# Optimization experiments

Measured on AMD Instinct MI355X. Metric: run time of the kernel, lower is better.

## Reference

```python
import jax, jax.numpy as jnp
import numpy as np

B, C_IN, FH, FW = 4, 256, 64, 176
N_PTS = 150000
D_BINS = 64
BEV_H = BEV_W = 200
RES = 0.5
EPS = 1e-5


def setup_inputs() -> dict:
    key = jax.random.key(0)
    ks = jax.random.split(key, 8)
    camera_features = jax.random.normal(ks[0], (B, C_IN, FH, FW), dtype=jnp.float32)
    pixels_uv = jax.random.uniform(ks[1], (B, N_PTS, 2), dtype=jnp.float32)
    K_inv = jax.random.normal(ks[2], (B, 3, 3), dtype=jnp.float32)
    # depth head params: Conv2d(256,128,3,pad=1) -> BN(128) -> ReLU -> Conv2d(128,64,1)
    W1 = jax.random.normal(ks[3], (128, C_IN, 3, 3), dtype=jnp.float32) * 0.02
    b1 = jnp.zeros((128,), dtype=jnp.float32)
    gamma = jnp.ones((128,), dtype=jnp.float32)
    beta = jnp.zeros((128,), dtype=jnp.float32)
    W2 = jax.random.normal(ks[4], (D_BINS, 128, 1, 1), dtype=jnp.float32) * 0.05
    b2 = jnp.zeros((D_BINS,), dtype=jnp.float32)
    depth_bins = jnp.linspace(1.0, 60.0, D_BINS, dtype=jnp.float32)
    return {"camera_features": camera_features, "pixels_uv": pixels_uv, "K_inv": K_inv,
            "W1": W1, "b1": b1, "gamma": gamma, "beta": beta, "W2": W2, "b2": b2,
            "depth_bins": depth_bins}


def _depth_head(x, W1, b1, gamma, beta, W2, b2):
    dn = ("NCHW", "OIHW", "NCHW")
    h = jax.lax.conv_general_dilated(x, W1, (1, 1), ((1, 1), (1, 1)), dimension_numbers=dn)
    h = h + b1[None, :, None, None]
    # BatchNorm2d, training-mode batch statistics (module is used without eval())
    mu = h.mean(axis=(0, 2, 3), keepdims=True)
    var = h.var(axis=(0, 2, 3), keepdims=True)
    h = (h - mu) * jax.lax.rsqrt(var + EPS)
    h = h * gamma[None, :, None, None] + beta[None, :, None, None]
    h = jax.nn.relu(h)
    logits = jax.lax.conv_general_dilated(h, W2, (1, 1), ((0, 0), (0, 0)), dimension_numbers=dn)
    logits = logits + b2[None, :, None, None]
    return jax.nn.softmax(logits, axis=1)  # [B, D, H, W]


def reference(camera_features, pixels_uv, K_inv, W1, b1, gamma, beta, W2, b2, depth_bins):
    depth_dist = _depth_head(camera_features, W1, b1, gamma, beta, W2, b2)

    # lift_to_3d
    exp_d = depth_dist.mean(axis=1)  # [B, H, W]
    ones = jnp.ones((B, N_PTS, 1), dtype=pixels_uv.dtype)
    homo = jnp.concatenate([pixels_uv, ones], axis=-1)            # [B, N, 3]
    pts3d = jnp.einsum('bnk,bjk->bnj', homo, K_inv)               # homo @ K_inv^T
    depth = exp_d.mean(axis=(1, 2))[:, None, None]                # [B, 1, 1]
    pts3d = pts3d * depth                                         # [B, N, 3]

    # splat_to_bev: scatter-add occupancy, then clamp to [0, 1]
    x_min = -(BEV_H * RES / 2)
    gx = jnp.clip(((pts3d[:, :, 0] - x_min) / RES).astype(jnp.int32), 0, BEV_W - 1)
    gy = jnp.clip(((pts3d[:, :, 1] - x_min) / RES).astype(jnp.int32), 0, BEV_H - 1)
    flat_idx = (jnp.arange(B, dtype=jnp.int32)[:, None] * (BEV_H * BEV_W) + gy * BEV_W + gx).ravel()
    grid = jnp.zeros((B * BEV_H * BEV_W,), dtype=jnp.float32).at[flat_idx].add(1.0)
    bev_grid = jnp.clip(grid.reshape(B, BEV_H, BEV_W), 0.0, 1.0)

    # expected_depth
    exp_depth = (depth_dist * depth_bins[None, :, None, None]).sum(axis=1)  # [B, H, W]

    return bev_grid, depth_dist, exp_depth, pts3d
```

## Files before the change

### kernel.cpp

```cpp
#include <hip/hip_runtime.h>

#define BATCH 4
#define CIN 256
#define FH 64
#define FW 176
#define HW (FH*FW)
#define PHW 11748
#define C1 128
#define DBINS 64
#define NPTS 150000
#define BEVN 200
#define EPSV 1e-5f

#define OFF_BEV 0
#define OFF_DD  160000
#define OFF_ED  3043584
#define OFF_PTS 3088640

#define WSB_H    0
#define WSB_WT   11534336
#define WSB_W2B  12124160
#define WSB_BN   12140544
#define WSB_XTP  12144640
#define XTP_B_ELEMS 3007488
#define WS_NEED_SPLIT 24174592ull

typedef short bfx8 __attribute__((ext_vector_type(8)));
typedef short bfx4 __attribute__((ext_vector_type(4)));
typedef float f32x4 __attribute__((ext_vector_type(4)));
typedef unsigned short u16;

__device__ __forceinline__ u16 f2bf(float f) {
  union { float f; unsigned int u; } v; v.f = f;
  unsigned int r = v.u + 0x7FFF + ((v.u >> 16) & 1);
  return (u16)(r >> 16);
}
__device__ __forceinline__ float bf2f(u16 h) {
  union { unsigned int u; float f; } v; v.u = ((unsigned int)h) << 16;
  return v.f;
}

__device__ __forceinline__ void gload_lds16(const void* g, void* l) {
  __builtin_amdgcn_global_load_lds(
      (const __attribute__((address_space(1))) unsigned int*)g,
      (__attribute__((address_space(3))) unsigned int*)l, 16, 0, 0);
}

__device__ __forceinline__ u16* xtp_base(u16* A, u16* B, int splitA, int bloc) {
  return (bloc < splitA) ? A + (size_t)bloc * XTP_B_ELEMS
                         : B + (size_t)(bloc - splitA) * XTP_B_ELEMS;
}

__global__ __launch_bounds__(256) void k_xt(
    const float* __restrict__ x, u16* __restrict__ xtpA,
    u16* __restrict__ xtpB, int splitA, int nbat,
    float* __restrict__ out, u16* __restrict__ w2b,
    const float* __restrict__ W2, u16* __restrict__ wt,
    const float* __restrict__ W1) {
  __shared__ u16 s_t[176 * 72];
  const int blk = blockIdx.x;
  const int t = threadIdx.x;
  const int idx = blk * 256 + t;

  if (idx < BATCH * BEVN * BEVN) out[OFF_BEV + idx] = 0.0f;
  if (idx < DBINS * C1) w2b[idx] = f2bf(W2[idx]);
  for (int i = idx; i < 9 * C1 * CIN; i += 262144) {
    int tap = i >> 15, rem = i & 32767;
    int co = rem >> 8, c = rem & 255;
    wt[i] = f2bf(W1[(co * CIN + c) * 9 + tap]);
  }
  const int nbord = nbat * 484 * 32;
  if (idx < nbord) {
    int bloc = idx / (484 * 32);
    int r = idx - bloc * 484 * 32;
    int bpx = r >> 5, ch8 = r & 31;
    int prow, pcol;
    if (bpx < 178)      { prow = 0;  pcol = bpx; }
    else if (bpx < 356) { prow = 65; pcol = bpx - 178; }
    else { int q = bpx - 356; prow = 1 + (q >> 1); pcol = (q & 1) * 177; }
    u16* xb = xtp_base(xtpA, xtpB, splitA, bloc);
    *(bfx8*)&xb[(prow * 178 + pcol) * 256 + ch8 * 8] = (bfx8)(short)0;
  }

  const int bloc = blk >> 8;
  const int rem = blk & 255;
  const int row = rem >> 2;
  const int c0 = (rem & 3) * 64;
  #pragma unroll
  for (int i = 0; i < 44; ++i) {
    int f = i * 256 + t;
    int c = f / 176, px = f - c * 176;
    s_t[px * 72 + c] = f2bf(x[((bloc * CIN + c0 + c) * FH + row) * FW + px]);
  }
  __syncthreads();
  u16* xb = xtp_base(xtpA, xtpB, splitA, bloc);
  const int base = ((row + 1) * 178 + 1) * 256 + c0;
  #pragma unroll
  for (int i = 0; i < 6; ++i) {
    int f = i * 256 + t;
    if (f < 1408) {
      int px = f >> 3, s = f & 7;
      *(bfx8*)&xb[base + (px << 8) + s * 8] = *(const bfx8*)&s_t[px * 72 + s * 8];
    }
  }
}

#define ABUF_E 4096
#define STEP_E 12288

__global__ __launch_bounds__(512) void k_conv(
    u16* __restrict__ xtpA, u16* __restrict__ xtpB, int splitA,
    const u16* __restrict__ wt, const float* __restrict__ b1,
    u16* __restrict__ hbf, int b0) {
  __shared__ __align__(16) u16 sMem[2 * STEP_E];

  const int blk = blockIdx.x;
  const int bloc = blk / 176;
  const int tile = blk % 176;
  const int h0 = (tile / 11) * 4;
  const int w0 = (tile % 11) * 16;
  const int b = b0 + bloc;
  const u16* xTp = xtp_base(xtpA, xtpB, splitA, bloc);
  const int t = threadIdx.x;
  const int lane = t & 63;
  const int wv = t >> 6;
  const int mw = wv >> 1, nw = wv & 1;
  const int l15 = lane & 15, kg = lane >> 4;

  int gA, gB0, gB1, ldA, ldB0, ldB1;
  {
    int c = t;
    int row = c >> 3;
    int slog = (c & 7) ^ (row & 7);
    int prow = h0 + (row >> 4), pcol = w0 + (row & 15);
    gA = (prow * 178 + pcol) * 256 + slog * 8;
    ldA = c * 8;
    gB0 = row * 256 + slog * 8;
    ldB0 = c * 8;
    c = t + 512; row = c >> 3;
    slog = (c & 7) ^ (row & 7);
    gB1 = row * 256 + slog * 8;
    ldB1 = c * 8;
  }

  f32x4 acc[4];
  #pragma unroll
  for (int nf = 0; nf < 4; ++nf) acc[nf] = (f32x4)(0.f);

#define STAGE(S, SEL)                                                          \
  {                                                                            \
    const int tap_ = (S) >> 2, cin0_ = ((S) & 3) << 6;                         \
    const int dy_ = tap_ / 3, dx_ = tap_ - dy_ * 3;                            \
    const int ao_ = ((dy_ * 178 + dx_) << 8) + cin0_;                          \
    const int wo_ = tap_ * 32768 + cin0_;                                      \
    u16* lb_ = &sMem[(SEL) * STEP_E];                                          \
    gload_lds16(&xTp[gA + ao_], &lb_[ldA]);                                    \
    gload_lds16(&wt[gB0 + wo_], &lb_[ABUF_E + ldB0]);                          \
    gload_lds16(&wt[gB1 + wo_], &lb_[ABUF_E + ldB1]);                          \
  }

#define COMPUTE(SEL)                                                           \
  {                                                                            \
    const u16* lb_ = &sMem[(SEL) * STEP_E];                                    \
    _Pragma("unroll")                                                          \
    for (int kk = 0; kk < 2; ++kk) {                                           \
      const int ph_ = (kk * 4 + kg) ^ (l15 & 7);                               \
      bfx8 af = *(const bfx8*)&lb_[(mw * 16 + l15) * 64 + ph_ * 8];            \
      bfx8 bf[4];                                                              \
      _Pragma("unroll")                                                        \
      for (int nf = 0; nf < 4; ++nf)                                           \
        bf[nf] = *(const bfx8*)&lb_[ABUF_E + (nw * 64 + nf * 16 + l15) * 64 + ph_ * 8]; \
      _Pragma("unroll")                                                        \
      for (int nf = 0; nf < 4; ++nf)                                           \
        acc[nf] = __builtin_amdgcn_mfma_f32_16x16x32_bf16(af, bf[nf], acc[nf], 0, 0, 0); \
    }                                                                          \
  }

#define VMCNT0 asm volatile("s_waitcnt vmcnt(0)" ::: "memory")
#define BARR __builtin_amdgcn_s_barrier()
#define SCHED0 __builtin_amdgcn_sched_barrier(0)

  STAGE(0, 0);

  #pragma unroll 1
  for (int s = 0; s < 36; s += 2) {
    VMCNT0; BARR; SCHED0;
    if (s + 1 < 36) STAGE(s + 1, 1);
    COMPUTE(0);
    VMCNT0; BARR; SCHED0;
    if (s + 2 < 36) STAGE(s + 2, 0);
    COMPUTE(1);
  }

  {
    const int py = h0 + mw;
    #pragma unroll
    for (int nf = 0; nf < 4; ++nf) {
      const int co = nw * 64 + nf * 16 + l15;
      const float bb = b1[co];
      bfx4 hv;
      #pragma unroll
      for (int j = 0; j < 4; ++j) hv[j] = (short)f2bf(acc[nf][j] + bb);
      *(bfx4*)&hbf[((b * C1 + co) * FH + py) * FW + w0 + kg * 4] = hv;
    }
  }
#undef STAGE
#undef COMPUTE
#undef VMCNT0
#undef BARR
#undef SCHED0
}

__global__ __launch_bounds__(256) void k_bnsum(
    const u16* __restrict__ h, float* __restrict__ part) {
  const int ch = blockIdx.x >> 2, b = blockIdx.x & 3;
  const int t = threadIdx.x;
  float s = 0.f, q = 0.f;
  const bfx8* p = (const bfx8*)&h[(b * C1 + ch) * HW];
  for (int i = t; i < HW / 8; i += 256) {
    bfx8 v8 = p[i];
    #pragma unroll
    for (int j = 0; j < 8; ++j) {
      float v = bf2f((u16)v8[j]);
      s += v;
      q = fmaf(v, v, q);
    }
  }
  #pragma unroll
  for (int o = 32; o; o >>= 1) {
    s += __shfl_xor(s, o);
    q += __shfl_xor(q, o);
  }
  __shared__ float rs[4], rq[4];
  int w = t >> 6;
  if ((t & 63) == 0) { rs[w] = s; rq[w] = q; }
  __syncthreads();
  if (t == 0) {
    part[ch * 8 + b * 2 + 0] = rs[0] + rs[1] + rs[2] + rs[3];
    part[ch * 8 + b * 2 + 1] = rq[0] + rq[1] + rq[2] + rq[3];
  }
}

__global__ __launch_bounds__(256) void k_head(
    const u16* __restrict__ h, const float* __restrict__ part,
    const float* __restrict__ gamma, const float* __restrict__ beta,
    const u16* __restrict__ w2b, const float* __restrict__ b2,
    const float* __restrict__ bins, float* __restrict__ out) {
  __shared__ u16 sAct[64 * 128];
  __shared__ float sP[64 * 68];
  __shared__ float sAB[256];

  const int blk = blockIdx.x;
  const int b = blk / 176;
  const int px0 = (blk % 176) * 64;
  const int t = threadIdx.x;
  const int lane = t & 63;
  const int w = t >> 6;
  const int l15 = lane & 15, kg = lane >> 4;

  if (t < 128) {
    float s = 0.f, q = 0.f;
    #pragma unroll
    for (int bb = 0; bb < 4; ++bb) {
      s += part[t * 8 + bb * 2 + 0];
      q += part[t * 8 + bb * 2 + 1];
    }
    const float inv_n = 1.0f / (float)(BATCH * HW);
    float mu = s * inv_n;
    float var = q * inv_n - mu * mu;
    float a = gamma[t] * rsqrtf(var + EPSV);
    sAB[t] = a;
    sAB[128 + t] = beta[t] - mu * a;
  }

  bfx8 bfr[4][4];
  #pragma unroll
  for (int nf = 0; nf < 4; ++nf)
    #pragma unroll
    for (int ck = 0; ck < 4; ++ck)
      bfr[nf][ck] = *(const bfx8*)&w2b[(nf * 16 + l15) * 128 + ck * 32 + kg * 8];
  float binr[4], b2r[4];
  #pragma unroll
  for (int nf = 0; nf < 4; ++nf) {
    binr[nf] = bins[nf * 16 + l15];
    b2r[nf] = b2[nf * 16 + l15];
  }
  f32x4 acc[4];
  #pragma unroll
  for (int nf = 0; nf < 4; ++nf) acc[nf] = (f32x4)(b2r[nf]);
  __syncthreads();

  #pragma unroll
  for (int i = 0; i < 4; ++i) {
    int f = t + i * 256;
    int c = f >> 3, g = f & 7;
    bfx8 v8 = *(const bfx8*)&h[(b * C1 + c) * HW + px0 + g * 8];
    float a = sAB[c], sh = sAB[128 + c];
    #pragma unroll
    for (int j = 0; j < 8; ++j) {
      int px = g * 8 + j;
      float v = fmaxf(fmaf(bf2f((u16)v8[j]), a, sh), 0.f);
      sAct[px * 128 + (((c >> 3) ^ (px & 15)) << 3) + (c & 7)] = f2bf(v);
    }
  }
  __syncthreads();

  #pragma unroll
  for (int ck = 0; ck < 4; ++ck) {
    bfx8 af = *(const bfx8*)&sAct[(w * 16 + l15) * 128 + (((ck * 4 + kg) ^ l15) << 3)];
    #pragma unroll
    for (int nf = 0; nf < 4; ++nf)
      acc[nf] = __builtin_amdgcn_mfma_f32_16x16x32_bf16(af, bfr[nf][ck], acc[nf], 0, 0, 0);
  }

  #pragma unroll
  for (int j = 0; j < 4; ++j) {
    float e[4];
    float z = 0.f, ez = 0.f;
    #pragma unroll
    for (int nf = 0; nf < 4; ++nf) {
      e[nf] = __expf(acc[nf][j]);
      z += e[nf];
      ez = fmaf(e[nf], binr[nf], ez);
    }
    #pragma unroll
    for (int o = 1; o < 16; o <<= 1) {
      z += __shfl_xor(z, o);
      ez += __shfl_xor(ez, o);
    }
    float inv = 1.0f / z;
    int px = w * 16 + kg * 4 + j;
    #pragma unroll
    for (int nf = 0; nf < 4; ++nf)
      sP[(nf * 16 + l15) * 68 + px] = e[nf] * inv;
    if (l15 == kg * 4 + j) out[OFF_ED + b * HW + px0 + px] = ez * inv;
  }
  __syncthreads();

  #pragma unroll
  for (int i = 0; i < 4; ++i) {
    int f = t + i * 256;
    int d = f >> 4, q = f & 15;
    f32x4 v;
    #pragma unroll
    for (int jj = 0; jj < 4; ++jj) v[jj] = sP[d * 68 + q * 4 + jj];
    *(f32x4*)&out[OFF_DD + (b * DBINS + d) * HW + px0 + q * 4] = v;
  }
}

__global__ void k_points(const float* __restrict__ uv, const float* __restrict__ kinv,
                         float* __restrict__ out) {
  int idx = blockIdx.x * 256 + threadIdx.x;
  if (idx >= BATCH * NPTS) return;
  int b = idx / NPTS;
  const float depth = 1.0f / 64.0f;
  float u = uv[idx * 2 + 0];
  float v = uv[idx * 2 + 1];
  const float* K = &kinv[b * 9];
  float p0 = (u * K[0] + v * K[1] + K[2]) * depth;
  float p1 = (u * K[3] + v * K[4] + K[5]) * depth;
  float p2 = (u * K[6] + v * K[7] + K[8]) * depth;
  out[OFF_PTS + idx * 3 + 0] = p0;
  out[OFF_PTS + idx * 3 + 1] = p1;
  out[OFF_PTS + idx * 3 + 2] = p2;
  int gx = (int)((p0 + 50.0f) * 2.0f);
  int gy = (int)((p1 + 50.0f) * 2.0f);
  gx = min(max(gx, 0), BEVN - 1);
  gy = min(max(gy, 0), BEVN - 1);
  out[OFF_BEV + (b * BEVN + gy) * BEVN + gx] = 1.0f;
}

extern "C" void kernel_launch(void* const* d_in, const int* in_sizes, int n_in,
                              void* d_out, int out_size, void* d_ws, size_t ws_size,
                              hipStream_t stream) {
  const float* x     = (const float*)d_in[0];
  const float* uv    = (const float*)d_in[1];
  const float* kinv  = (const float*)d_in[2];
  const float* w1    = (const float*)d_in[3];
  const float* b1    = (const float*)d_in[4];
  const float* gamma = (const float*)d_in[5];
  const float* beta  = (const float*)d_in[6];
  const float* w2    = (const float*)d_in[7];
  const float* b2    = (const float*)d_in[8];
  const float* bins  = (const float*)d_in[9];
  float* out = (float*)d_out;

  u16*   wsH   = (u16*)d_ws;
  u16*   wsWT  = (u16*)((char*)d_ws + WSB_WT);
  u16*   wsW2B = (u16*)((char*)d_ws + WSB_W2B);
  float* wsBN  = (float*)((char*)d_ws + WSB_BN);
  u16*   wsXTP = (u16*)((char*)d_ws + WSB_XTP);
  u16*   doXTP = (u16*)(out + OFF_DD);

  if (ws_size >= WS_NEED_SPLIT) {
    k_xt<<<1024, 256, 0, stream>>>(x, wsXTP, doXTP, 2, 4, out, wsW2B, w2, wsWT, w1);
    k_conv<<<704, 512, 0, stream>>>(wsXTP, doXTP, 2, wsWT, b1, wsH, 0);
  } else {
    for (int b0 = 0; b0 < BATCH; ++b0) {
      k_xt<<<256, 256, 0, stream>>>(x + (size_t)b0 * CIN * HW, wsXTP, wsXTP, 1,
                                    (b0 == 0) ? 1 : 0, out, wsW2B, w2, wsWT, w1);
      k_conv<<<176, 512, 0, stream>>>(wsXTP, wsXTP, 1, wsWT, b1, wsH, b0);
    }
  }
  k_bnsum<<<512, 256, 0, stream>>>(wsH, wsBN);
  k_head<<<704, 256, 0, stream>>>(wsH, wsBN, gamma, beta, wsW2B, b2, bins, out);
  k_points<<<(BATCH * NPTS + 255) / 256, 256, 0, stream>>>(uv, kinv, out);
}
```

Before: 80.84 us.

## Fuse BatchNorm statistics into conv epilogue and vectorize transpose loads

The conv kernel's epilogue now computes per-channel sum and sum-of-squares from the fp32 accumulators, reduces them across waves in shared memory, and writes per-tile partials to scratch space placed inside the output buffer. A small k_bnred kernel then sums the 704 tile partials per channel, replacing k_bnsum, which re-read the whole bf16 activation tensor. Statistics now come from fp32 values instead of rounded bf16, which slightly changes numerics. The input transpose kernel also switches to float4 global loads. The scratch region sits at the tail of the output buffer and must be overwritten later, which is a correctness risk.

```diff
diff --git a/kernel.cpp b/kernel.cpp
--- a/kernel.cpp
+++ b/kernel.cpp
@@ -16,6 +16,7 @@
 #define OFF_DD  160000
 #define OFF_ED  3043584
 #define OFF_PTS 3088640
+#define OFF_P2  3167488
 
 #define WSB_H    0
 #define WSB_WT   11534336
@@ -87,10 +88,12 @@
   const int row = rem >> 2;
   const int c0 = (rem & 3) * 64;
   #pragma unroll
-  for (int i = 0; i < 44; ++i) {
+  for (int i = 0; i < 11; ++i) {
     int f = i * 256 + t;
-    int c = f / 176, px = f - c * 176;
-    s_t[px * 72 + c] = f2bf(x[((bloc * CIN + c0 + c) * FH + row) * FW + px]);
+    int c = f / 44, p4 = (f - c * 44) * 4;
+    const f32x4 v = *(const f32x4*)&x[((bloc * CIN + c0 + c) * FH + row) * FW + p4];
+    #pragma unroll
+    for (int j = 0; j < 4; ++j) s_t[(p4 + j) * 72 + c] = f2bf(v[j]);
   }
   __syncthreads();
   u16* xb = xtp_base(xtpA, xtpB, splitA, bloc);
@@ -111,7 +114,7 @@
 __global__ __launch_bounds__(512) void k_conv(
     u16* __restrict__ xtpA, u16* __restrict__ xtpB, int splitA,
     const u16* __restrict__ wt, const float* __restrict__ b1,
-    u16* __restrict__ hbf, int b0) {
+    u16* __restrict__ hbf, float* __restrict__ part2, int tgof, int b0) {
   __shared__ __align__(16) u16 sMem[2 * STEP_E];
 
   const int blk = blockIdx.x;
@@ -194,14 +197,45 @@
 
   {
     const int py = h0 + mw;
+    float ps[4], pq[4];
     #pragma unroll
     for (int nf = 0; nf < 4; ++nf) {
       const int co = nw * 64 + nf * 16 + l15;
       const float bb = b1[co];
       bfx4 hv;
+      float s = 0.f, q = 0.f;
       #pragma unroll
-      for (int j = 0; j < 4; ++j) hv[j] = (short)f2bf(acc[nf][j] + bb);
+      for (int j = 0; j < 4; ++j) {
+        float v = acc[nf][j] + bb;
+        hv[j] = (short)f2bf(v);
+        s += v;
+        q = fmaf(v, v, q);
+      }
+      ps[nf] = s; pq[nf] = q;
       *(bfx4*)&hbf[((b * C1 + co) * FH + py) * FW + w0 + kg * 4] = hv;
+    }
+    BARR;
+    float* red = (float*)sMem;
+    #pragma unroll
+    for (int nf = 0; nf < 4; ++nf) {
+      float s = ps[nf], q = pq[nf];
+      s += __shfl_xor(s, 16); s += __shfl_xor(s, 32);
+      q += __shfl_xor(q, 16); q += __shfl_xor(q, 32);
+      if (lane < 16) {
+        int ridx = ((mw * 2 + nw) * 4 + nf) * 16 + lane;
+        red[ridx] = s;
+        red[512 + ridx] = q;
+      }
+    }
+    BARR;
+    if (t < 256) {
+      int sq = t & 1, l = (t >> 1) & 15, nf2 = (t >> 5) & 3, nw2 = t >> 7;
+      float sum = 0.f;
+      #pragma unroll
+      for (int m = 0; m < 4; ++m)
+        sum += red[sq * 512 + ((m * 2 + nw2) * 4 + nf2) * 16 + l];
+      int co = nw2 * 64 + nf2 * 16 + l;
+      part2[(size_t)(tgof + blk) * 256 + co * 2 + sq] = sum;
     }
   }
 #undef STAGE
@@ -211,20 +245,14 @@
 #undef SCHED0
 }
 
-__global__ __launch_bounds__(256) void k_bnsum(
-    const u16* __restrict__ h, float* __restrict__ part) {
-  const int ch = blockIdx.x >> 2, b = blockIdx.x & 3;
+__global__ __launch_bounds__(256) void k_bnred(
+    const float* __restrict__ part2, float* __restrict__ part, int ntiles) {
+  const int ch = blockIdx.x;
   const int t = threadIdx.x;
   float s = 0.f, q = 0.f;
-  const bfx8* p = (const bfx8*)&h[(b * C1 + ch) * HW];
-  for (int i = t; i < HW / 8; i += 256) {
-    bfx8 v8 = p[i];
-    #pragma unroll
-    for (int j = 0; j < 8; ++j) {
-      float v = bf2f((u16)v8[j]);
-      s += v;
-      q = fmaf(v, v, q);
-    }
+  for (int tile = t; tile < ntiles; tile += 256) {
+    s += part2[(size_t)tile * 256 + ch * 2 + 0];
+    q += part2[(size_t)tile * 256 + ch * 2 + 1];
   }
   #pragma unroll
   for (int o = 32; o; o >>= 1) {
@@ -236,8 +264,8 @@
   if ((t & 63) == 0) { rs[w] = s; rq[w] = q; }
   __syncthreads();
   if (t == 0) {
-    part[ch * 8 + b * 2 + 0] = rs[0] + rs[1] + rs[2] + rs[3];
-    part[ch * 8 + b * 2 + 1] = rq[0] + rq[1] + rq[2] + rq[3];
+    part[ch * 2 + 0] = rs[0] + rs[1] + rs[2] + rs[3];
+    part[ch * 2 + 1] = rq[0] + rq[1] + rq[2] + rq[3];
   }
 }
 
@@ -259,12 +287,8 @@
   const int l15 = lane & 15, kg = lane >> 4;
 
   if (t < 128) {
-    float s = 0.f, q = 0.f;
-    #pragma unroll
-    for (int bb = 0; bb < 4; ++bb) {
-      s += part[t * 8 + bb * 2 + 0];
-      q += part[t * 8 + bb * 2 + 1];
-    }
+    float s = part[t * 2 + 0];
+    float q = part[t * 2 + 1];
     const float inv_n = 1.0f / (float)(BATCH * HW);
     float mu = s * inv_n;
     float var = q * inv_n - mu * mu;
@@ -391,18 +415,20 @@
   float* wsBN  = (float*)((char*)d_ws + WSB_BN);
   u16*   wsXTP = (u16*)((char*)d_ws + WSB_XTP);
   u16*   doXTP = (u16*)(out + OFF_DD);
+  float* part2 = out + OFF_P2;
 
   if (ws_size >= WS_NEED_SPLIT) {
     k_xt<<<1024, 256, 0, stream>>>(x, wsXTP, doXTP, 2, 4, out, wsW2B, w2, wsWT, w1);
-    k_conv<<<704, 512, 0, stream>>>(wsXTP, doXTP, 2, wsWT, b1, wsH, 0);
+    k_conv<<<704, 512, 0, stream>>>(wsXTP, doXTP, 2, wsWT, b1, wsH, part2, 0, 0);
   } else {
     for (int b0 = 0; b0 < BATCH; ++b0) {
       k_xt<<<256, 256, 0, stream>>>(x + (size_t)b0 * CIN * HW, wsXTP, wsXTP, 1,
                                     (b0 == 0) ? 1 : 0, out, wsW2B, w2, wsWT, w1);
-      k_conv<<<176, 512, 0, stream>>>(wsXTP, wsXTP, 1, wsWT, b1, wsH, b0);
-    }
-  }
-  k_bnsum<<<512, 256, 0, stream>>>(wsH, wsBN);
+      k_conv<<<176, 512, 0, stream>>>(wsXTP, wsXTP, 1, wsWT, b1, wsH,
+                                      part2, b0 * 176, b0);
+    }
+  }
+  k_bnred<<<128, 256, 0, stream>>>(part2, wsBN, 704);
   k_head<<<704, 256, 0, stream>>>(wsH, wsBN, gamma, beta, wsW2B, b2, bins, out);
   k_points<<<(BATCH * NPTS + 255) / 256, 256, 0, stream>>>(uv, kinv, out);
 }
```

Result: slower. 83.23 us (+3.0%).
